# Performance work log

Measured on AMD Instinct MI355X. Metric: run time of the kernel, lower is better.

Reference implementation:

```python
import jax, jax.numpy as jnp
import numpy as np

N_NODES = 100000
N_EDGES = 1600000
IN_CH, EDGE_DIM, HIDDEN, OUT_CH = 3, 3, 64, 1


def setup_inputs() -> dict:
    key = jax.random.key(0)
    ks = jax.random.split(key, 10)
    x = jax.random.normal(ks[0], (N_NODES, IN_CH), dtype=jnp.float32)
    edge_index = jax.random.randint(ks[1], (2, N_EDGES), 0, N_NODES, dtype=jnp.int64)
    edge_attr = jax.random.normal(ks[2], (N_EDGES, EDGE_DIM), dtype=jnp.float32)
    # Linear params (torch Linear: y = x @ W.T + b); we store W as (in, out)
    s1 = 1.0 / np.sqrt(IN_CH + EDGE_DIM)
    W1 = jax.random.uniform(ks[3], (IN_CH + EDGE_DIM, HIDDEN), jnp.float32, -s1, s1)
    b1 = jax.random.uniform(ks[4], (HIDDEN,), jnp.float32, -s1, s1)
    s2 = 1.0 / np.sqrt(HIDDEN + EDGE_DIM)
    W2 = jax.random.uniform(ks[5], (HIDDEN + EDGE_DIM, HIDDEN), jnp.float32, -s2, s2)
    b2 = jax.random.uniform(ks[6], (HIDDEN,), jnp.float32, -s2, s2)
    s3 = 1.0 / np.sqrt(HIDDEN)
    W3 = jax.random.uniform(ks[7], (HIDDEN, OUT_CH), jnp.float32, -s3, s3)
    b3 = jax.random.uniform(ks[8], (OUT_CH,), jnp.float32, -s3, s3)
    return {"x": x, "edge_index": edge_index, "edge_attr": edge_attr,
            "W1": W1, "b1": b1, "W2": W2, "b2": b2, "W3": W3, "b3": b3}


def _edge_conv(h, src, dst, edge_attr, W, b, n_nodes):
    # gather source node features, concat edge_attr, linear, scatter-add at dst
    msg = jnp.concatenate([h[src], edge_attr], axis=-1) @ W + b  # [E, out]
    return jax.ops.segment_sum(msg, dst, num_segments=n_nodes)   # [N, out]


def reference(x, edge_index, edge_attr, W1, b1, W2, b2, W3, b3):
    src, dst = edge_index[0], edge_index[1]  # PyG source_to_target: aggregate at edge_index[1]
    n = x.shape[0]
    h = jax.nn.relu(_edge_conv(x, src, dst, edge_attr, W1, b1, n))
    h = jax.nn.relu(_edge_conv(h, src, dst, edge_attr, W2, b2, n))
    return h @ W3 + b3  # (n_nodes, 1) anomaly logits
```

## Files before the change

kernel.cpp:

```cpp
#include <hip/hip_runtime.h>

#define N_NODES 100000
#define N_EDGES 1600000
#define NCHUNK 256
#define CHUNK_E (N_EDGES / NCHUNK)
#define BSHIFT 6
#define BMASK 63
#define NBUCK 1563
#define REC_CAP 1536


typedef unsigned int uint4_ev __attribute__((ext_vector_type(4)));
typedef short bf16x8 __attribute__((ext_vector_type(8)));
typedef float f32x4 __attribute__((ext_vector_type(4)));

__device__ __forceinline__ unsigned short f2bf(float f) {
    unsigned int u = __float_as_uint(f);
    unsigned int r = (u + 0x7fff + ((u >> 16) & 1)) >> 16;
    return (unsigned short)r;
}
__device__ __forceinline__ unsigned int pack2bf(float a, float b) {
    return (unsigned int)f2bf(a) | ((unsigned int)f2bf(b) << 16);
}
__device__ __forceinline__ float bflo(unsigned int v) { return __uint_as_float(v << 16); }
__device__ __forceinline__ float bfhi(unsigned int v) { return __uint_as_float(v & 0xffff0000u); }

__device__ __forceinline__ float4 nt_load4(const float4* p) {
    uint4_ev v = __builtin_nontemporal_load((const uint4_ev*)p);
    return make_float4(__uint_as_float(v.x), __uint_as_float(v.y),
                       __uint_as_float(v.z), __uint_as_float(v.w));
}

__device__ __forceinline__ int wave_incl_scan(int v, int lane) {
#pragma unroll
    for (int off = 1; off < 64; off <<= 1) {
        int t = __shfl_up(v, off, 64);
        if (lane >= off) v += t;
    }
    return v;
}

__global__ __launch_bounds__(1024) void k_hist(const int* __restrict__ ei,
                                               int* __restrict__ tbl,
                                               const float* __restrict__ W2,
                                               unsigned short* __restrict__ wpk) {
    if (blockIdx.x == NCHUNK) {
        int i = threadIdx.x;
        if (i < 512) {
            int lane = i & 63, hh = (i >> 6) & 1, nt = i >> 7;
            int col = nt * 16 + (lane & 15);
            int k0 = hh * 32 + (lane >> 4) * 8;
#pragma unroll
            for (int j = 0; j < 8; j++)
                wpk[i * 8 + j] = f2bf(W2[(k0 + j) * 64 + col]);
        }
        return;
    }
    __shared__ int h[NBUCK];
    for (int i = threadIdx.x; i < NBUCK; i += 1024) h[i] = 0;
    __syncthreads();
    const int base = blockIdx.x * CHUNK_E;
    for (int i = threadIdx.x; i < CHUNK_E; i += 1024)
        atomicAdd(&h[ei[N_EDGES + base + i] >> BSHIFT], 1);
    __syncthreads();
    for (int i = threadIdx.x; i < NBUCK; i += 1024)
        tbl[blockIdx.x * NBUCK + i] = h[i];
}

__global__ __launch_bounds__(256) void k_colscan(int* __restrict__ tbl,
                                                 int* __restrict__ bsum) {
    const int b = blockIdx.x, t = threadIdx.x;
    int v = tbl[t * NBUCK + b];
    int lane = t & 63, w = t >> 6;
    int inc = wave_incl_scan(v, lane);
    __shared__ int ws[4];
    if (lane == 63) ws[w] = inc;
    __syncthreads();
    int wo = 0;
    for (int k = 0; k < w; k++) wo += ws[k];
    tbl[t * NBUCK + b] = wo + inc - v;
    if (t == 255) bsum[b] = wo + inc;
}

__global__ __launch_bounds__(1024) void k_basescan(const int* __restrict__ bsum,
                                                   int* __restrict__ bbase) {
    int t = threadIdx.x, lane = t & 63, w = t >> 6;
    int i0 = 2 * t, i1 = 2 * t + 1;
    int v0 = (i0 < NBUCK) ? bsum[i0] : 0;
    int v1 = (i1 < NBUCK) ? bsum[i1] : 0;
    int s = v0 + v1;
    int inc = wave_incl_scan(s, lane);
    __shared__ int ws[16];
    if (lane == 63) ws[w] = inc;
    __syncthreads();
    int wo = 0;
    for (int k = 0; k < w; k++) wo += ws[k];
    int excl = wo + inc - s;
    if (i0 < NBUCK) bbase[i0] = excl;
    if (i1 < NBUCK) bbase[i1] = excl + v0;
    if (i0 == NBUCK - 1) bbase[NBUCK] = excl + v0;
}

__global__ __launch_bounds__(1024) void k_scatter(const int* __restrict__ ei,
                                                  const float* __restrict__ ea,
                                                  const int* __restrict__ tbl,
                                                  const int* __restrict__ bbase,
                                                  float4* __restrict__ stg) {
    __shared__ int cur[NBUCK];
    for (int i = threadIdx.x; i < NBUCK; i += 1024)
        cur[i] = tbl[blockIdx.x * NBUCK + i] + bbase[i];
    __syncthreads();
    const int base = blockIdx.x * CHUNK_E;
    for (int i = threadIdx.x; i < CHUNK_E; i += 1024) {
        int e = base + i;
        int src = ei[e];
        int dst = ei[N_EDGES + e];
        float a0 = ea[(size_t)e * 3 + 0];
        float a1 = ea[(size_t)e * 3 + 1];
        float a2 = ea[(size_t)e * 3 + 2];
        int p = atomicAdd(&cur[dst >> BSHIFT], 1);
        unsigned pk = (unsigned)src | ((unsigned)(dst & BMASK) << 17);
        stg[p] = make_float4(__uint_as_float(pk), a0, a1, a2);
    }
}

__global__ __launch_bounds__(256) void k_finalize(
    const float4* __restrict__ stg, const int* __restrict__ bbase,
    const float* __restrict__ x, const float* __restrict__ W1,
    const float* __restrict__ b1, const float* __restrict__ W2,
    const float* __restrict__ b2, const bf16x8* __restrict__ wpk,
    int* __restrict__ csr, int* __restrict__ degp, int* __restrict__ rowend,
    unsigned int* __restrict__ zu, unsigned int* __restrict__ eu) {
    __shared__ float4 rec[REC_CAP];
    __shared__ int hist[64], lofs[64], cur[64];
    __shared__ float sU[64 * 3], sT[64 * 3];
    const int b = blockIdx.x, t = threadIdx.x;
    const int base = bbase[b], cnt = bbase[b + 1] - base;
    if (t < 64) hist[t] = 0;
    __syncthreads();
    const float* stgf = (const float*)stg;
    for (int i = t; i < cnt; i += 256) {
        unsigned pk = __float_as_uint(stgf[(size_t)(base + i) * 4]);
        atomicAdd(&hist[pk >> 17], 1);
    }
    __syncthreads();
    if (t < 64) {
        int v = hist[t];
        int inc = wave_incl_scan(v, t);
        lofs[t] = inc - v;
        cur[t] = inc - v;
    }
    __syncthreads();
    for (int i = t; i < cnt; i += 256) {
        float4 r = nt_load4(&stg[base + i]);
        unsigned pk = __float_as_uint(r.x);
        int p = atomicAdd(&cur[pk >> 17], 1);
        if (p < REC_CAP) rec[p] = r;
    }
    __syncthreads();
    {
        const int l = t >> 2, sub = t & 3;
        const int n = b * 64 + l;
        const int d = hist[l], lo = lofs[l];
        float u0 = 0, u1 = 0, u2 = 0, t0 = 0, t1 = 0, t2 = 0;
        for (int j = sub; j < d; j += 4) {
            float4 r = rec[lo + j];
            unsigned pk = __float_as_uint(r.x);
            int src = pk & 0x1FFFF;
            csr[base + lo + j] = src;
            t0 += r.y; t1 += r.z; t2 += r.w;
            u0 += x[src * 3 + 0]; u1 += x[src * 3 + 1]; u2 += x[src * 3 + 2];
        }
#pragma unroll
        for (int off = 1; off <= 2; off <<= 1) {
            u0 += __shfl_xor(u0, off, 64); u1 += __shfl_xor(u1, off, 64);
            u2 += __shfl_xor(u2, off, 64); t0 += __shfl_xor(t0, off, 64);
            t1 += __shfl_xor(t1, off, 64); t2 += __shfl_xor(t2, off, 64);
        }
        if (sub == 0) {
            sU[l * 3 + 0] = u0; sU[l * 3 + 1] = u1; sU[l * 3 + 2] = u2;
            sT[l * 3 + 0] = t0; sT[l * 3 + 1] = t1; sT[l * 3 + 2] = t2;
            if (n < N_NODES) {
                degp[n] = d;
                rowend[n] = base + lo + d;
            }
        }
    }
    __syncthreads();
    const int lane = t & 63, w = t >> 6;
    const int tb = b * 64 + w * 16;
    if (tb >= N_NODES) return;
    const int col = lane & 15;
    const int q = lane >> 4;
    const int ln = w * 16 + col;
    const float d = (float)hist[ln];
    const float u0 = sU[ln * 3], u1 = sU[ln * 3 + 1], u2 = sU[ln * 3 + 2];
    const float t0 = sT[ln * 3], t1 = sT[ln * 3 + 1], t2 = sT[ln * 3 + 2];
    bf16x8 af[2];
#pragma unroll
    for (int h = 0; h < 2; h++) {
#pragma unroll
        for (int j = 0; j < 8; j++) {
            int c = h * 32 + q * 8 + j;
            float a = d * b1[c];
            a = fmaf(u0, W1[0 * 64 + c], a);
            a = fmaf(u1, W1[1 * 64 + c], a);
            a = fmaf(u2, W1[2 * 64 + c], a);
            a = fmaf(t0, W1[3 * 64 + c], a);
            a = fmaf(t1, W1[4 * 64 + c], a);
            a = fmaf(t2, W1[5 * 64 + c], a);
            af[h][j] = (short)f2bf(fmaxf(a, 0.f));
        }
    }
    f32x4 acc[4];
#pragma unroll
    for (int nt = 0; nt < 4; nt++) {
        bf16x8 b0 = wpk[(nt * 2 + 0) * 64 + lane];
        bf16x8 b1f = wpk[(nt * 2 + 1) * 64 + lane];
        f32x4 a = {0.f, 0.f, 0.f, 0.f};
        a = __builtin_amdgcn_mfma_f32_16x16x32_bf16(af[0], b0, a, 0, 0, 0);
        a = __builtin_amdgcn_mfma_f32_16x16x32_bf16(af[1], b1f, a, 0, 0, 0);
        acc[nt] = a;
    }
#pragma unroll
    for (int nt = 0; nt < 4; nt++) {
#pragma unroll
        for (int r = 0; r < 4; r++) {
            float v = acc[nt][r];
            float pv = __shfl_xor(v, 1, 64);
            if ((lane & 1) == 0) {
                int nr = tb + q * 4 + r;
                zu[(size_t)nr * 32 + nt * 8 + (col >> 1)] = pack2bf(v, pv);
            }
        }
    }
    const float eb = b2[lane];
    const float w64 = W2[64 * 64 + lane];
    const float w65 = W2[65 * 64 + lane];
    const float w66 = W2[66 * 64 + lane];
#pragma unroll 4
    for (int mm = 0; mm < 16; mm++) {
        int lm = w * 16 + mm;
        float dd = (float)hist[lm];
        float s0 = sT[lm * 3], s1 = sT[lm * 3 + 1], s2 = sT[lm * 3 + 2];
        float e = dd * eb;
        e = fmaf(s0, w64, e); e = fmaf(s1, w65, e); e = fmaf(s2, w66, e);
        float pe = __shfl_xor(e, 1, 64);
        if ((lane & 1) == 0)
            eu[(size_t)(tb + mm) * 32 + (lane >> 1)] = pack2bf(e, pe);
    }
}

__global__ __launch_bounds__(256) void k_agg(
    const unsigned int* __restrict__ zu, const unsigned int* __restrict__ eu,
    const int* __restrict__ rowend, const int* __restrict__ degp,
    const int* __restrict__ csr, const float* __restrict__ W3,
    const float* __restrict__ b3, float* __restrict__ out) {
    const int lane = threadIdx.x & 63;
    const int li = lane & 15;
    const int q = li & 7;
    const int r = li >> 3;
    const int n = blockIdx.x * 16 + (threadIdx.x >> 4);

    float cw3[8];
#pragma unroll
    for (int m = 0; m < 8; m++) cw3[m] = W3[8 * q + m];
    const float b3v = b3[0];

    const int end = rowend[n], d = degp[n], start = end - d;
    float S[8];
#pragma unroll
    for (int m = 0; m < 8; m++) S[m] = 0.f;

    for (int c = start; c < end; c += 16) {
        int idx[8];
        float mk[8];
        uint4 v[8];
#pragma unroll
        for (int u = 0; u < 8; u++) {
            int i = c + 2 * u + r;
            bool ok = i < end;
            mk[u] = ok ? 1.f : 0.f;
            idx[u] = csr[ok ? i : start];
        }
#pragma unroll
        for (int u = 0; u < 8; u++)
            v[u] = *(const uint4*)&zu[(size_t)idx[u] * 32 + q * 4];
#pragma unroll
        for (int u = 0; u < 8; u++) {
            S[0] = fmaf(mk[u], bflo(v[u].x), S[0]); S[1] = fmaf(mk[u], bfhi(v[u].x), S[1]);
            S[2] = fmaf(mk[u], bflo(v[u].y), S[2]); S[3] = fmaf(mk[u], bfhi(v[u].y), S[3]);
            S[4] = fmaf(mk[u], bflo(v[u].z), S[4]); S[5] = fmaf(mk[u], bfhi(v[u].z), S[5]);
            S[6] = fmaf(mk[u], bflo(v[u].w), S[6]); S[7] = fmaf(mk[u], bfhi(v[u].w), S[7]);
        }
    }
#pragma unroll
    for (int m = 0; m < 8; m++) S[m] += __shfl_xor(S[m], 8, 64);

    const uint4 ev = *(const uint4*)&eu[(size_t)n * 32 + q * 4];
    float contrib;
    {
        float h0 = fmaxf(S[0] + bflo(ev.x), 0.f);
        float h1v = fmaxf(S[1] + bfhi(ev.x), 0.f);
        float h2v = fmaxf(S[2] + bflo(ev.y), 0.f);
        float h3 = fmaxf(S[3] + bfhi(ev.y), 0.f);
        float h4 = fmaxf(S[4] + bflo(ev.z), 0.f);
        float h5 = fmaxf(S[5] + bfhi(ev.z), 0.f);
        float h6 = fmaxf(S[6] + bflo(ev.w), 0.f);
        float h7 = fmaxf(S[7] + bfhi(ev.w), 0.f);
        contrib = h0 * cw3[0];
        contrib = fmaf(h1v, cw3[1], contrib);
        contrib = fmaf(h2v, cw3[2], contrib);
        contrib = fmaf(h3, cw3[3], contrib);
        contrib = fmaf(h4, cw3[4], contrib);
        contrib = fmaf(h5, cw3[5], contrib);
        contrib = fmaf(h6, cw3[6], contrib);
        contrib = fmaf(h7, cw3[7], contrib);
    }
    contrib += __shfl_xor(contrib, 1, 64);
    contrib += __shfl_xor(contrib, 2, 64);
    contrib += __shfl_xor(contrib, 4, 64);
    if (li == 0) out[n] = contrib + b3v;
}

extern "C" void kernel_launch(void* const* d_in, const int* in_sizes, int n_in,
                              void* d_out, int out_size, void* d_ws, size_t ws_size,
                              hipStream_t stream) {
    const float* x  = (const float*)d_in[0];
    const int*   ei = (const int*)d_in[1];
    const float* ea = (const float*)d_in[2];
    const float* W1 = (const float*)d_in[3];
    const float* b1 = (const float*)d_in[4];
    const float* W2 = (const float*)d_in[5];
    const float* b2 = (const float*)d_in[6];
    const float* W3 = (const float*)d_in[7];
    const float* b3 = (const float*)d_in[8];
    float* out = (float*)d_out;

    char* ws = (char*)d_ws;
    int*    tbl    = (int*)(ws + 0);
    int*    bsum   = (int*)(ws + 1600512);
    int*    bbase  = (int*)(ws + 1606912);
    int*    degp   = (int*)(ws + 1613312);
    int*    rowend = (int*)(ws + 2013440);
    int*    csr    = (int*)(ws + 2413568);
    float4* stg    = (float4*)(ws + 8813568);
    unsigned int* zu = (unsigned int*)(ws + 34413568);
    unsigned int* eu = (unsigned int*)(ws + 47213568);
    unsigned short* wpk = (unsigned short*)(ws + 60013568);

    k_hist<<<NCHUNK + 1, 1024, 0, stream>>>(ei, tbl, W2, wpk);
    k_colscan<<<NBUCK, 256, 0, stream>>>(tbl, bsum);
    k_basescan<<<1, 1024, 0, stream>>>(bsum, bbase);
    k_scatter<<<NCHUNK, 1024, 0, stream>>>(ei, ea, tbl, bbase, stg);
    k_finalize<<<NBUCK, 256, 0, stream>>>(stg, bbase, x, W1, b1, W2, b2,
                                          (const bf16x8*)wpk, csr, degp, rowend, zu, eu);
    k_agg<<<N_NODES / 16, 256, 0, stream>>>(zu, eu, rowend, degp, csr, W3, b3, out);
}
```

Before: 185.6 us.

## Replace bucketed two-level counting sort with per-node global-atomic CSR build

Swaps the chunked histogram, column scan and local in-block re-sort for a direct per-node degree count done with global atomics, followed by a bucket-level scan and per-node row-start scan. The scatter step then places each edge at its exact CSR slot through a global atomic cursor, so finalize reads edges straight from global memory without a shared-memory resort. This removes two kernels, the large per-chunk table and LDS sorting work. The cost is heavy contention on global atomics across 1.6M edges, plus an added memset and a small kernel, and CSR order within a row is no longer deterministic.

Measured after the change: 342.5 us. +84.6%, slower.

```diff
diff --git a/kernel.cpp b/kernel.cpp
--- a/kernel.cpp
+++ b/kernel.cpp
@@ -4,10 +4,8 @@
 #define N_EDGES 1600000
 #define NCHUNK 256
 #define CHUNK_E (N_EDGES / NCHUNK)
-#define BSHIFT 6
-#define BMASK 63
 #define NBUCK 1563
-#define REC_CAP 1536
+#define NP 100032
 
 
 typedef unsigned int uint4_ev __attribute__((ext_vector_type(4)));
@@ -40,10 +38,10 @@
     return v;
 }
 
-__global__ __launch_bounds__(1024) void k_hist(const int* __restrict__ ei,
-                                               int* __restrict__ tbl,
-                                               const float* __restrict__ W2,
-                                               unsigned short* __restrict__ wpk) {
+__global__ __launch_bounds__(1024) void k_deg(const int* __restrict__ ei,
+                                              int* __restrict__ degp,
+                                              const float* __restrict__ W2,
+                                              unsigned short* __restrict__ wpk) {
     if (blockIdx.x == NCHUNK) {
         int i = threadIdx.x;
         if (i < 512) {
@@ -56,38 +54,26 @@
         }
         return;
     }
-    __shared__ int h[NBUCK];
-    for (int i = threadIdx.x; i < NBUCK; i += 1024) h[i] = 0;
-    __syncthreads();
     const int base = blockIdx.x * CHUNK_E;
     for (int i = threadIdx.x; i < CHUNK_E; i += 1024)
-        atomicAdd(&h[ei[N_EDGES + base + i] >> BSHIFT], 1);
-    __syncthreads();
-    for (int i = threadIdx.x; i < NBUCK; i += 1024)
-        tbl[blockIdx.x * NBUCK + i] = h[i];
-}
-
-__global__ __launch_bounds__(256) void k_colscan(int* __restrict__ tbl,
-                                                 int* __restrict__ bsum) {
-    const int b = blockIdx.x, t = threadIdx.x;
-    int v = tbl[t * NBUCK + b];
-    int lane = t & 63, w = t >> 6;
-    int inc = wave_incl_scan(v, lane);
-    __shared__ int ws[4];
-    if (lane == 63) ws[w] = inc;
-    __syncthreads();
-    int wo = 0;
-    for (int k = 0; k < w; k++) wo += ws[k];
-    tbl[t * NBUCK + b] = wo + inc - v;
-    if (t == 255) bsum[b] = wo + inc;
-}
-
-__global__ __launch_bounds__(1024) void k_basescan(const int* __restrict__ bsum,
+        atomicAdd(&degp[ei[N_EDGES + base + i]], 1);
+}
+
+__global__ __launch_bounds__(1024) void k_basescan(const int* __restrict__ degp,
                                                    int* __restrict__ bbase) {
     int t = threadIdx.x, lane = t & 63, w = t >> 6;
     int i0 = 2 * t, i1 = 2 * t + 1;
-    int v0 = (i0 < NBUCK) ? bsum[i0] : 0;
-    int v1 = (i1 < NBUCK) ? bsum[i1] : 0;
+    int v0 = 0, v1 = 0;
+    if (i0 < NBUCK) {
+        const int4* p = (const int4*)&degp[i0 << 6];
+#pragma unroll
+        for (int k = 0; k < 16; k++) { int4 q = p[k]; v0 += q.x + q.y + q.z + q.w; }
+    }
+    if (i1 < NBUCK) {
+        const int4* p = (const int4*)&degp[i1 << 6];
+#pragma unroll
+        for (int k = 0; k < 16; k++) { int4 q = p[k]; v1 += q.x + q.y + q.z + q.w; }
+    }
     int s = v0 + v1;
     int inc = wave_incl_scan(s, lane);
     __shared__ int ws[16];
@@ -101,15 +87,22 @@
     if (i0 == NBUCK - 1) bbase[NBUCK] = excl + v0;
 }
 
+__global__ __launch_bounds__(1024) void k_rowstart(const int* __restrict__ degp,
+                                                   const int* __restrict__ bbase,
+                                                   int* __restrict__ cursor) {
+    const int lane = threadIdx.x & 63, w = threadIdx.x >> 6;
+    const int g = blockIdx.x * 16 + w;
+    if (g >= NBUCK) return;
+    const int n = g * 64 + lane;
+    int d = (n < N_NODES) ? degp[n] : 0;
+    int inc = wave_incl_scan(d, lane);
+    if (n < N_NODES) cursor[n] = bbase[g] + inc - d;
+}
+
 __global__ __launch_bounds__(1024) void k_scatter(const int* __restrict__ ei,
                                                   const float* __restrict__ ea,
-                                                  const int* __restrict__ tbl,
-                                                  const int* __restrict__ bbase,
+                                                  int* __restrict__ cursor,
                                                   float4* __restrict__ stg) {
-    __shared__ int cur[NBUCK];
-    for (int i = threadIdx.x; i < NBUCK; i += 1024)
-        cur[i] = tbl[blockIdx.x * NBUCK + i] + bbase[i];
-    __syncthreads();
     const int base = blockIdx.x * CHUNK_E;
     for (int i = threadIdx.x; i < CHUNK_E; i += 1024) {
         int e = base + i;
@@ -118,44 +111,29 @@
         float a0 = ea[(size_t)e * 3 + 0];
         float a1 = ea[(size_t)e * 3 + 1];
         float a2 = ea[(size_t)e * 3 + 2];
-        int p = atomicAdd(&cur[dst >> BSHIFT], 1);
-        unsigned pk = (unsigned)src | ((unsigned)(dst & BMASK) << 17);
-        stg[p] = make_float4(__uint_as_float(pk), a0, a1, a2);
+        int p = atomicAdd(&cursor[dst], 1);
+        stg[p] = make_float4(__uint_as_float((unsigned)src), a0, a1, a2);
     }
 }
 
 __global__ __launch_bounds__(256) void k_finalize(
     const float4* __restrict__ stg, const int* __restrict__ bbase,
-    const float* __restrict__ x, const float* __restrict__ W1,
-    const float* __restrict__ b1, const float* __restrict__ W2,
-    const float* __restrict__ b2, const bf16x8* __restrict__ wpk,
-    int* __restrict__ csr, int* __restrict__ degp, int* __restrict__ rowend,
-    unsigned int* __restrict__ zu, unsigned int* __restrict__ eu) {
-    __shared__ float4 rec[REC_CAP];
-    __shared__ int hist[64], lofs[64], cur[64];
+    const int* __restrict__ degp, const float* __restrict__ x,
+    const float* __restrict__ W1, const float* __restrict__ b1,
+    const float* __restrict__ W2, const float* __restrict__ b2,
+    const bf16x8* __restrict__ wpk, int* __restrict__ csr,
+    int* __restrict__ rowend, unsigned int* __restrict__ zu,
+    unsigned int* __restrict__ eu) {
+    __shared__ int hist[64], lofs[64];
     __shared__ float sU[64 * 3], sT[64 * 3];
     const int b = blockIdx.x, t = threadIdx.x;
-    const int base = bbase[b], cnt = bbase[b + 1] - base;
-    if (t < 64) hist[t] = 0;
-    __syncthreads();
-    const float* stgf = (const float*)stg;
-    for (int i = t; i < cnt; i += 256) {
-        unsigned pk = __float_as_uint(stgf[(size_t)(base + i) * 4]);
-        atomicAdd(&hist[pk >> 17], 1);
-    }
-    __syncthreads();
+    const int base = bbase[b];
     if (t < 64) {
-        int v = hist[t];
-        int inc = wave_incl_scan(v, t);
-        lofs[t] = inc - v;
-        cur[t] = inc - v;
-    }
-    __syncthreads();
-    for (int i = t; i < cnt; i += 256) {
-        float4 r = nt_load4(&stg[base + i]);
-        unsigned pk = __float_as_uint(r.x);
-        int p = atomicAdd(&cur[pk >> 17], 1);
-        if (p < REC_CAP) rec[p] = r;
+        int n = b * 64 + t;
+        int d = (n < N_NODES) ? degp[n] : 0;
+        hist[t] = d;
+        int inc = wave_incl_scan(d, t);
+        lofs[t] = inc - d;
     }
     __syncthreads();
     {
@@ -164,9 +142,8 @@
         const int d = hist[l], lo = lofs[l];
         float u0 = 0, u1 = 0, u2 = 0, t0 = 0, t1 = 0, t2 = 0;
         for (int j = sub; j < d; j += 4) {
-            float4 r = rec[lo + j];
-            unsigned pk = __float_as_uint(r.x);
-            int src = pk & 0x1FFFF;
+            float4 r = nt_load4(&stg[base + lo + j]);
+            int src = (int)__float_as_uint(r.x);
             csr[base + lo + j] = src;
             t0 += r.y; t1 += r.z; t2 += r.w;
             u0 += x[src * 3 + 0]; u1 += x[src * 3 + 1]; u2 += x[src * 3 + 2];
@@ -180,10 +157,7 @@
         if (sub == 0) {
             sU[l * 3 + 0] = u0; sU[l * 3 + 1] = u1; sU[l * 3 + 2] = u2;
             sT[l * 3 + 0] = t0; sT[l * 3 + 1] = t1; sT[l * 3 + 2] = t2;
-            if (n < N_NODES) {
-                degp[n] = d;
-                rowend[n] = base + lo + d;
-            }
+            if (n < N_NODES) rowend[n] = base + lo + d;
         }
     }
     __syncthreads();
@@ -338,22 +312,22 @@
     float* out = (float*)d_out;
 
     char* ws = (char*)d_ws;
-    int*    tbl    = (int*)(ws + 0);
-    int*    bsum   = (int*)(ws + 1600512);
-    int*    bbase  = (int*)(ws + 1606912);
-    int*    degp   = (int*)(ws + 1613312);
-    int*    rowend = (int*)(ws + 2013440);
-    int*    csr    = (int*)(ws + 2413568);
-    float4* stg    = (float4*)(ws + 8813568);
-    unsigned int* zu = (unsigned int*)(ws + 34413568);
-    unsigned int* eu = (unsigned int*)(ws + 47213568);
-    unsigned short* wpk = (unsigned short*)(ws + 60013568);
-
-    k_hist<<<NCHUNK + 1, 1024, 0, stream>>>(ei, tbl, W2, wpk);
-    k_colscan<<<NBUCK, 256, 0, stream>>>(tbl, bsum);
-    k_basescan<<<1, 1024, 0, stream>>>(bsum, bbase);
-    k_scatter<<<NCHUNK, 1024, 0, stream>>>(ei, ea, tbl, bbase, stg);
-    k_finalize<<<NBUCK, 256, 0, stream>>>(stg, bbase, x, W1, b1, W2, b2,
-                                          (const bf16x8*)wpk, csr, degp, rowend, zu, eu);
+    int*    degp   = (int*)(ws + 0);
+    int*    bbase  = (int*)(ws + 400384);
+    int*    cursor = (int*)(ws + 406784);
+    int*    rowend = (int*)(ws + 807168);
+    int*    csr    = (int*)(ws + 1207552);
+    float4* stg    = (float4*)(ws + 7607552);
+    unsigned int* zu = (unsigned int*)(ws + 33207552);
+    unsigned int* eu = (unsigned int*)(ws + 46007552);
+    unsigned short* wpk = (unsigned short*)(ws + 58807552);
+
+    hipMemsetAsync(degp, 0, NP * sizeof(int), stream);
+    k_deg<<<NCHUNK + 1, 1024, 0, stream>>>(ei, degp, W2, wpk);
+    k_basescan<<<1, 1024, 0, stream>>>(degp, bbase);
+    k_rowstart<<<98, 1024, 0, stream>>>(degp, bbase, cursor);
+    k_scatter<<<NCHUNK, 1024, 0, stream>>>(ei, ea, cursor, stg);
+    k_finalize<<<NBUCK, 256, 0, stream>>>(stg, bbase, degp, x, W1, b1, W2, b2,
+                                          (const bf16x8*)wpk, csr, rowend, zu, eu);
     k_agg<<<N_NODES / 16, 256, 0, stream>>>(zu, eu, rowend, degp, csr, W3, b3, out);
 }
```
